# Optimization experiments

Hardware: AMD Instinct MI355X
Metric: run time of the kernel (lower is better)

## Reference

```python
import jax, jax.numpy as jnp
import numpy as np

B, KVH, HPK, D = 4, 8, 4, 128          # batch, n_kv_heads, n_heads_per_kv, head_size
SEQ_KV = 4096                           # cached history length
SEQ = SEQ_KV + 1                        # history + current token
K, LOCAL_K, SINK, RANK = 512, 128, 4, 32


def gather(t, axis, i):
    """Broadcasting take_along_axis, mirroring the torch `gather` helper."""
    axis = axis % t.ndim
    tgt = list(t.shape)
    tgt[axis] = i.shape[axis]
    return jnp.take_along_axis(t, jnp.broadcast_to(i, tgt), axis)


def sparse_q_score(q, key_cpu_t, cur_key_t):
    # q: (B,KVH,HPK,1,D); key_cpu_t: (B,KVH,D,SEQ_KV); cur_key_t: (B,KVH,1,D,1)
    absq = jnp.abs(q).sum(2, keepdims=True)                    # (B,KVH,1,1,D)
    _, idx = jax.lax.top_k(absq, RANK)                         # (B,KVH,1,1,RANK)
    q_proj = gather(q, -1, idx)                                # (B,KVH,HPK,1,RANK)
    idx_t = jnp.swapaxes(idx, -1, -2)                          # (B,KVH,1,RANK,1)
    k_hist = gather(key_cpu_t[:, :, None], -2, idx_t)          # (B,KVH,1,RANK,SEQ_KV)
    k_cur = gather(cur_key_t, -2, idx_t)                       # (B,KVH,1,RANK,1)
    k_proj = jnp.concatenate([k_hist, k_cur], -1)              # (B,KVH,1,RANK,SEQ)
    scale = jnp.sqrt(jnp.abs(q_proj).sum(-1) / jnp.abs(q).sum(-1) * D)[..., None]
    return jnp.matmul(q_proj, k_proj) / scale                  # (B,KVH,HPK,1,SEQ)


def setup_inputs():
    key = jax.random.key(0)
    ks = jax.random.split(key, 6)
    query = jax.random.normal(ks[0], (B, KVH * HPK, 1, D), jnp.float32)
    k = jax.random.normal(ks[1], (B, KVH, 1, D), jnp.float32)
    v = jax.random.normal(ks[2], (B, KVH, 1, D), jnp.float32)
    logmask = jnp.zeros((B, KVH * HPK, 1, SEQ), jnp.float32)
    key_cpu = jax.random.normal(ks[3], (B, KVH, SEQ_KV, D), jnp.float32)
    value_cpu = jax.random.normal(ks[4], (B, KVH, SEQ_KV, D), jnp.float32)
    s_key_cpu = jnp.swapaxes(key_cpu, -1, -2)                  # head-size-contiguous copy
    mean_v = jax.random.normal(ks[5], (B, KVH, 1, 1, D), jnp.float32)
    return {"query": query, "key": k, "value": v, "logmask": logmask,
            "key_cpu": key_cpu, "value_cpu": value_cpu,
            "s_key_cpu": s_key_cpu, "mean_v": mean_v}


def reference(query, key, value, logmask, key_cpu, value_cpu, s_key_cpu, mean_v):
    q = query.reshape(B, KVH, HPK, 1, D)
    k = key.reshape(B, KVH, 1, 1, D)
    v = value.reshape(B, KVH, 1, 1, D)
    lm = logmask.reshape(B, KVH, HPK, 1, SEQ)
    # approximate scores over the full key history + current key
    score = (sparse_q_score(q, s_key_cpu, jnp.swapaxes(k, 3, 4)) + lm).astype(jnp.float32)
    # causal index over history (excluding current token): 0 = most recent unmasked
    neg = jnp.isneginf(lm[..., :-1])
    ci = jnp.where(neg, -1,
                   jnp.cumsum((~neg)[..., ::-1].astype(jnp.int32), -1)[..., ::-1] - 1)
    is_local = (0 <= ci) & (ci < LOCAL_K)
    is_sink = ci >= SEQ - SINK - 1
    fmax = jnp.finfo(jnp.float32).max
    topk_score = jnp.where(is_local | is_sink, fmax, score[..., :-1]).sum(2, keepdims=True)
    kk = min(K + SINK, SEQ)
    _, indices = jax.lax.top_k(topk_score, kk)                 # (B,KVH,1,1,kk)
    # running mean value update
    mean_v_new = (mean_v * (SEQ - 1) + v.astype(jnp.float32)) / SEQ
    # weight reallocation to the mean value
    norm = jax.nn.softmax(score, -1)
    kv_weight = gather(norm, -1, indices).sum(-1) + norm[..., -1]  # (B,KVH,HPK,1)
    # gather selected K/V and append current token
    kv_idx = indices[..., 0, :, None]                          # (B,KVH,1,kk,1)
    key_g = jnp.concatenate([gather(key_cpu[:, :, None], -2, kv_idx), k], -2)   # (B,KVH,1,kk+1,D)
    val_g = jnp.concatenate([gather(value_cpu[:, :, None], -2, kv_idx), v], -2)
    cur_idx = jnp.full(indices.shape[:-1] + (1,), SEQ - 1, indices.dtype)
    lm_g = gather(lm, -1, jnp.concatenate([indices, cur_idx], -1))  # (B,KVH,HPK,1,kk+1)
    # dense attention over the reduced key set
    scores = jnp.matmul(q, jnp.swapaxes(key_g, -1, -2)) * (D ** -0.5) + lm_g
    weights = jax.nn.softmax(scores.astype(jnp.float32), -1) * kv_weight[..., None]
    out = jnp.matmul(weights, val_g) + (1.0 - kv_weight[..., None]) * mean_v_new
    return out.reshape(B, KVH * HPK, 1, D), weights.reshape(B, KVH * HPK, 1, kk + 1)
```

## Files before the change

### kernel.cpp

```cpp
#include <hip/hip_runtime.h>
#include <math.h>

#define NBH 32
#define HPKN 4
#define DN 128
#define SEQKV 4096
#define SEQN 4097
#define SSTR 4100
#define RANKN 32
#define KSEL 516
#define SINKN 4
#define LOCALK 128
#define NMASK 132
#define NTOP 384
#define NCHUNK 16

__global__ __launch_bounds__(256) void k2_scores(
    const float* __restrict__ q, const float* __restrict__ key,
    const float* __restrict__ skey, const float* __restrict__ lm,
    float* __restrict__ scores, float* __restrict__ tk,
    float2* __restrict__ partials) {
  int bh = blockIdx.y;
  int s0 = blockIdx.x << 8;
  int t = threadIdx.x;
  int wave = t >> 6, lane = t & 63;
  __shared__ float qv[4][128];
  __shared__ float absq[128];
  __shared__ int sel[RANKN];
  __shared__ float qp[4][RANKN];
  __shared__ float wred[4][4];

  {
    float v0 = q[(size_t)bh * 512 + t];
    float v1 = q[(size_t)bh * 512 + 256 + t];
    qv[t >> 7][t & 127] = v0;
    qv[2 + (t >> 7)][t & 127] = v1;
  }
  __syncthreads();
  if (t < 128)
    absq[t] = fabsf(qv[0][t]) + fabsf(qv[1][t]) + fabsf(qv[2][t]) + fabsf(qv[3][t]);
  __syncthreads();
  if (t < 128) {
    float a = absq[t];
    int rank = 0;
    for (int e = 0; e < 128; ++e) {
      float ae = absq[e];
      rank += (ae > a) || (ae == a && e < t);
    }
    if (rank < RANKN) sel[rank] = t;
  }
  __syncthreads();
  {
    float fa = fabsf(qv[wave][lane]) + fabsf(qv[wave][lane + 64]);
    for (int off = 32; off > 0; off >>= 1) fa += __shfl_down(fa, off);
    float full = __shfl(fa, 0);
    float qsel = (lane < RANKN) ? qv[wave][sel[lane]] : 0.f;
    float sv = fabsf(qsel);
    for (int off = 32; off > 0; off >>= 1) sv += __shfl_down(sv, off);
    float selsum = __shfl(sv, 0);
    float scale = sqrtf(selsum / full * 128.f);
    if (lane < RANKN) qp[wave][lane] = qsel / scale;
  }
  __syncthreads();

  if (blockIdx.x == 0) {
    float kv = (lane < RANKN) ? key[bh * 128 + sel[lane]] : 0.f;
    float pr = (lane < RANKN) ? qp[wave][lane] * kv : 0.f;
    for (int off = 32; off > 0; off >>= 1) pr += __shfl_down(pr, off);
    if (lane == 0)
      scores[(size_t)(bh * 4 + wave) * SSTR + SEQKV] =
          pr + lm[(size_t)(bh * 4 + wave) * SEQN + SEQKV];
  }

  const float* kb = skey + (size_t)bh * 128 * 4096;
  float a0 = 0, a1 = 0, a2 = 0, a3 = 0;
#pragma unroll 8
  for (int r = 0; r < RANKN; ++r) {
    float k0 = kb[((size_t)sel[r] << 12) + s0 + t];
    a0 += qp[0][r] * k0;
    a1 += qp[1][r] * k0;
    a2 += qp[2][r] * k0;
    a3 += qp[3][r] * k0;
  }
  float sc[4];
  {
    int s = s0 + t;
    sc[0] = a0 + lm[(size_t)(bh * 4 + 0) * SEQN + s];
    sc[1] = a1 + lm[(size_t)(bh * 4 + 1) * SEQN + s];
    sc[2] = a2 + lm[(size_t)(bh * 4 + 2) * SEQN + s];
    sc[3] = a3 + lm[(size_t)(bh * 4 + 3) * SEQN + s];
    float sum = sc[0] + sc[1] + sc[2] + sc[3];
#pragma unroll
    for (int p = 0; p < 4; ++p)
      scores[(size_t)(bh * 4 + p) * SSTR + s] = sc[p];
    tk[(bh << 12) + s] = sum;
  }

#pragma unroll
  for (int p = 0; p < 4; ++p) {
    float mx = sc[p];
    for (int off = 32; off > 0; off >>= 1) mx = fmaxf(mx, __shfl_down(mx, off));
    if (lane == 0) wred[wave][p] = mx;
  }
  __syncthreads();
  float bm[4];
#pragma unroll
  for (int p = 0; p < 4; ++p)
    bm[p] = fmaxf(fmaxf(wred[0][p], wred[1][p]), fmaxf(wred[2][p], wred[3][p]));
  __syncthreads();
#pragma unroll
  for (int p = 0; p < 4; ++p) {
    float e = expf(sc[p] - bm[p]);
    for (int off = 32; off > 0; off >>= 1) e += __shfl_down(e, off);
    if (lane == 0) wred[wave][p] = e;
  }
  __syncthreads();
  if (t < 4) {
    float s = wred[0][t] + wred[1][t] + wred[2][t] + wred[3][t];
    partials[(size_t)(bh * 4 + t) * NCHUNK + blockIdx.x] = make_float2(bm[t], s);
  }
}

__global__ __launch_bounds__(256) void k3_topk(
    const float* __restrict__ tk, int* __restrict__ indices) {
  int bh = blockIdx.x;
  int t = threadIdx.x;
  int lane = t & 63;
  __shared__ unsigned us[4096];
  __shared__ unsigned hist[2048];
  __shared__ unsigned long long binlist[2048];
  __shared__ unsigned long long selk[512];
  __shared__ unsigned chunkSum[32];
  __shared__ int c1, c2, binB_s, nAbove_s, needed_s;

  {
    const float4* tk4 = (const float4*)(tk + (bh << 12));
    for (int i = t; i < 1024; i += 256) {
      float4 v = tk4[i];
      unsigned b0 = __float_as_uint(v.x), b1 = __float_as_uint(v.y);
      unsigned b2 = __float_as_uint(v.z), b3 = __float_as_uint(v.w);
      us[i * 4 + 0] = (b0 & 0x80000000u) ? ~b0 : (b0 | 0x80000000u);
      us[i * 4 + 1] = (b1 & 0x80000000u) ? ~b1 : (b1 | 0x80000000u);
      us[i * 4 + 2] = (b2 & 0x80000000u) ? ~b2 : (b2 | 0x80000000u);
      us[i * 4 + 3] = (b3 & 0x80000000u) ? ~b3 : (b3 | 0x80000000u);
    }
  }
  for (int i = t; i < 2048; i += 256) hist[i] = 0;
  if (t == 0) { c1 = 0; c2 = 0; }
  __syncthreads();

  for (int s = SINKN + t; s < SEQKV - LOCALK; s += 256)
    atomicAdd(&hist[us[s] >> 21], 1u);
  __syncthreads();

  if (t < 32) {
    unsigned sum = 0;
    for (int i = 0; i < 64; ++i) sum += hist[t * 64 + i];
    chunkSum[t] = sum;
  }
  __syncthreads();

  if (t < 64) {
    int l = t;
    unsigned x = (l < 32) ? chunkSum[l] : 0;
    unsigned sfx = x;
    for (int off = 1; off < 64; off <<= 1) {
      unsigned y = __shfl_down(sfx, off);
      if (l + off < 64) sfx += y;
    }
    unsigned above = sfx - x;
    bool hit = (l < 32) && (above < NTOP) && (above + x >= NTOP);
    unsigned long long mask = __ballot(hit);
    int C = __ffsll(mask) - 1;
    unsigned aboveC = __shfl(above, C);
    unsigned h = hist[C * 64 + l];
    unsigned sfx2 = h;
    for (int off = 1; off < 64; off <<= 1) {
      unsigned y = __shfl_down(sfx2, off);
      if (l + off < 64) sfx2 += y;
    }
    unsigned above2 = aboveC + (sfx2 - h);
    bool hit2 = (above2 < NTOP) && (above2 + h >= NTOP);
    unsigned long long mask2 = __ballot(hit2);
    int lB = __ffsll(mask2) - 1;
    if (l == lB) {
      binB_s = C * 64 + l;
      nAbove_s = (int)above2;
      needed_s = NTOP - (int)above2;
    }
  }
  __syncthreads();
  unsigned B = (unsigned)binB_s;
  int nAbove = nAbove_s, needed = needed_s;

  for (int s0 = SINKN; s0 < SEQKV - LOCALK; s0 += 256) {
    int s = s0 + t;
    bool valid = (s < SEQKV - LOCALK);
    unsigned u = valid ? us[s] : 0u;
    unsigned bin = u >> 21;
    bool win = valid && (bin > B);
    bool bnd = valid && (bin == B);
    unsigned long long mw = __ballot(win);
    unsigned long long mb = __ballot(bnd);
    int bw = 0, bb = 0;
    if (lane == 0) {
      if (mw) bw = atomicAdd(&c1, __popcll(mw));
      if (mb) bb = atomicAdd(&c2, __popcll(mb));
    }
    bw = __shfl(bw, 0);
    bb = __shfl(bb, 0);
    unsigned long long lmask = (1ULL << lane) - 1ULL;
    unsigned long long key = ((unsigned long long)u << 32) | (unsigned)(~s);
    if (win) selk[bw + __popcll(mw & lmask)] = key;
    if (bnd) {
      int pos = bb + __popcll(mb & lmask);
      if (pos < 2048) binlist[pos] = key;
    }
  }
  __syncthreads();
  int m2 = c2;
  int p2 = 1;
  while (p2 < m2) p2 <<= 1;
  for (int i = m2 + t; i < p2; i += 256) binlist[i] = 0ULL;
  __syncthreads();
  for (int k = 2; k <= p2; k <<= 1)
    for (int j = k >> 1; j > 0; j >>= 1) {
      for (int i = t; i < p2; i += 256) {
        int ixj = i ^ j;
        if (ixj > i) {
          bool desc = ((i & k) == 0);
          unsigned long long a = binlist[i], bb2 = binlist[ixj];
          if ((a < bb2) == desc) { binlist[i] = bb2; binlist[ixj] = a; }
        }
      }
      __syncthreads();
    }
  for (int i = t; i < needed; i += 256) selk[nAbove + i] = binlist[i];
  for (int i = NTOP + t; i < 512; i += 256) selk[i] = 0ULL;
  __syncthreads();

  unsigned long long e0 = selk[t], e1 = selk[t + 256];
  int i1 = t + 256;
  for (int k = 2; k <= 512; k <<= 1) {
    for (int j = k >> 1; j > 0; j >>= 1) {
      if (j == 256) {
        if (e0 < e1) { unsigned long long tmp = e0; e0 = e1; e1 = tmp; }
      } else if (j >= 64) {
        selk[t] = e0; selk[i1] = e1;
        __syncthreads();
        unsigned long long p0 = selk[t ^ j], p1 = selk[i1 ^ j];
        __syncthreads();
        bool d0 = ((t & k) == 0), l0 = ((t & j) == 0);
        e0 = (d0 == l0) ? (e0 > p0 ? e0 : p0) : (e0 < p0 ? e0 : p0);
        bool d1 = ((i1 & k) == 0), l1 = ((i1 & j) == 0);
        e1 = (d1 == l1) ? (e1 > p1 ? e1 : p1) : (e1 < p1 ? e1 : p1);
      } else {
        unsigned long long p0 = __shfl_xor(e0, j);
        unsigned long long p1 = __shfl_xor(e1, j);
        bool d0 = ((t & k) == 0), l0 = ((t & j) == 0);
        e0 = (d0 == l0) ? (e0 > p0 ? e0 : p0) : (e0 < p0 ? e0 : p0);
        bool d1 = ((i1 & k) == 0);
        e1 = (d1 == l0) ? (e1 > p1 ? e1 : p1) : (e1 < p1 ? e1 : p1);
      }
    }
  }

  if (t < SINKN) indices[bh * KSEL + t] = t;
  for (int i = t; i < LOCALK; i += 256)
    indices[bh * KSEL + SINKN + i] = (SEQKV - LOCALK) + i;
  indices[bh * KSEL + NMASK + t] = (int)(~(unsigned)(e0 & 0xFFFFFFFFu));
  if (t < NTOP - 256)
    indices[bh * KSEL + NMASK + 256 + t] = (int)(~(unsigned)(e1 & 0xFFFFFFFFu));
}

__global__ __launch_bounds__(512) void kC_tail(
    const float* __restrict__ q, const float* __restrict__ key,
    const float* __restrict__ value, const float* __restrict__ lm,
    const float* __restrict__ key_cpu, const float* __restrict__ value_cpu,
    const float* __restrict__ mean_v, const float* __restrict__ scores,
    const float2* __restrict__ partials, const int* __restrict__ indices,
    float* __restrict__ out, float* __restrict__ out_w) {
  const int bh = blockIdx.x;
  const int t = threadIdx.x;
  const int wave = t >> 6, lane = t & 63;
  const int grp = lane >> 4, gl = lane & 15;

  __shared__ int sidxs[520];
  __shared__ float qv[512];
  __shared__ float s2s[4 * 520];
  __shared__ float ws2[4 * 520];
  __shared__ float redA[8], redB[8], redC[8];

  qv[t] = q[((size_t)bh << 9) + t];
  for (int j = t; j < KSEL; j += 512) sidxs[j] = indices[bh * KSEL + j];
  __syncthreads();

  {
    const float rsqd = 0.08838834764831845f;
    const float4* qv4 = (const float4*)qv;
    float4 qA[4], qB[4];
#pragma unroll
    for (int p = 0; p < 4; ++p) {
      qA[p] = qv4[p * 32 + gl * 2];
      qB[p] = qv4[p * 32 + gl * 2 + 1];
    }
    for (int r = 0; r < 17; ++r) {
      int j = (r << 5) + (wave << 2) + grp;
      if (j <= KSEL) {
        int sj = (j < KSEL) ? sidxs[j] : SEQKV;
        const float* krow = (j < KSEL)
            ? key_cpu + ((((size_t)bh << 12) + sj) << 7)
            : key + ((size_t)bh << 7);
        const float4* k4 = (const float4*)krow;
        float4 kA = k4[gl * 2], kB = k4[gl * 2 + 1];
        float d0 = qA[0].x * kA.x + qA[0].y * kA.y + qA[0].z * kA.z + qA[0].w * kA.w +
                   qB[0].x * kB.x + qB[0].y * kB.y + qB[0].z * kB.z + qB[0].w * kB.w;
        float d1 = qA[1].x * kA.x + qA[1].y * kA.y + qA[1].z * kA.z + qA[1].w * kA.w +
                   qB[1].x * kB.x + qB[1].y * kB.y + qB[1].z * kB.z + qB[1].w * kB.w;
        float d2 = qA[2].x * kA.x + qA[2].y * kA.y + qA[2].z * kA.z + qA[2].w * kA.w +
                   qB[2].x * kB.x + qB[2].y * kB.y + qB[2].z * kB.z + qB[2].w * kB.w;
        float d3 = qA[3].x * kA.x + qA[3].y * kA.y + qA[3].z * kA.z + qA[3].w * kA.w +
                   qB[3].x * kB.x + qB[3].y * kB.y + qB[3].z * kB.z + qB[3].w * kB.w;
        for (int off = 8; off > 0; off >>= 1) {
          d0 += __shfl_down(d0, off);
          d1 += __shfl_down(d1, off);
          d2 += __shfl_down(d2, off);
          d3 += __shfl_down(d3, off);
        }
        if (gl == 0) {
          size_t lmb = (size_t)(bh * 4) * SEQN + sj;
          s2s[0 * 520 + j] = d0 * rsqd + lm[lmb + 0 * SEQN];
          s2s[1 * 520 + j] = d1 * rsqd + lm[lmb + 1 * SEQN];
          s2s[2 * 520 + j] = d2 * rsqd + lm[lmb + 2 * SEQN];
          s2s[3 * 520 + j] = d3 * rsqd + lm[lmb + 3 * SEQN];
        }
      }
    }
  }
  __syncthreads();

  const int p = t >> 7, tt = t & 127;
  const int qw = tt >> 6;
  const int bhp = bh * 4 + p;
  float kvw;
  {
    const float* srow = scores + (size_t)bhp * SSTR;
    float cur = srow[SEQKV];

    float m = cur, sumexp;
    {
      float2 pc[NCHUNK];
#pragma unroll
      for (int c = 0; c < NCHUNK; ++c) {
        pc[c] = partials[(size_t)bhp * NCHUNK + c];
        m = fmaxf(m, pc[c].x);
      }
      float s = expf(cur - m);
#pragma unroll
      for (int c = 0; c < NCHUNK; ++c) s += pc[c].y * expf(pc[c].x - m);
      sumexp = s;
    }

    float ss = 0.f;
    for (int j = tt; j < KSEL; j += 128) ss += expf(srow[sidxs[j]] - m);
    for (int off = 32; off > 0; off >>= 1) ss += __shfl_down(ss, off);
    if (lane == 0) redA[p * 2 + qw] = ss;
    __syncthreads();
    float sstot = redA[p * 2] + redA[p * 2 + 1];
    kvw = (sstot + expf(cur - m)) / sumexp;

    float mx = -INFINITY;
    for (int j = tt; j < KSEL + 1; j += 128) mx = fmaxf(mx, s2s[p * 520 + j]);
    for (int off = 32; off > 0; off >>= 1) mx = fmaxf(mx, __shfl_down(mx, off));
    if (lane == 0) redB[p * 2 + qw] = mx;
    __syncthreads();
    float m2 = fmaxf(redB[p * 2], redB[p * 2 + 1]);
    float se = 0.f;
    for (int j = tt; j < KSEL + 1; j += 128) se += expf(s2s[p * 520 + j] - m2);
    for (int off = 32; off > 0; off >>= 1) se += __shfl_down(se, off);
    if (lane == 0) redC[p * 2 + qw] = se;
    __syncthreads();
    float inv = kvw / (redC[p * 2] + redC[p * 2 + 1]);

    for (int j = tt; j < KSEL + 1; j += 128) {
      float w = expf(s2s[p * 520 + j] - m2) * inv;
      ws2[p * 520 + j] = w;
      out_w[(size_t)bhp * (KSEL + 1) + j] = w;
    }
  }
  __syncthreads();

  {
    const int d = tt;
    float vcur = value[((size_t)bh << 7) + d];
    float mvn = (mean_v[((size_t)bh << 7) + d] * 4096.f + vcur) / 4097.f;
    float a0 = (1.f - kvw) * mvn, a1 = 0.f, a2 = 0.f, a3 = 0.f;
    const float* vbase = value_cpu + ((size_t)bh << 19);
    for (int j = 0; j < KSEL; j += 4) {
      int s0 = sidxs[j], s1 = sidxs[j + 1], s2i = sidxs[j + 2], s3 = sidxs[j + 3];
      a0 += ws2[p * 520 + j] * vbase[((size_t)s0 << 7) + d];
      a1 += ws2[p * 520 + j + 1] * vbase[((size_t)s1 << 7) + d];
      a2 += ws2[p * 520 + j + 2] * vbase[((size_t)s2i << 7) + d];
      a3 += ws2[p * 520 + j + 3] * vbase[((size_t)s3 << 7) + d];
    }
    a0 += ws2[p * 520 + KSEL] * vcur;
    out[((size_t)bhp << 7) + d] = (a0 + a1) + (a2 + a3);
  }
}

extern "C" void kernel_launch(void* const* d_in, const int* in_sizes, int n_in,
                              void* d_out, int out_size, void* d_ws, size_t ws_size,
                              hipStream_t stream) {
  const float* query     = (const float*)d_in[0];
  const float* key       = (const float*)d_in[1];
  const float* value     = (const float*)d_in[2];
  const float* logmask   = (const float*)d_in[3];
  const float* key_cpu   = (const float*)d_in[4];
  const float* value_cpu = (const float*)d_in[5];
  const float* s_key_cpu = (const float*)d_in[6];
  const float* mean_v    = (const float*)d_in[7];

  float* out   = (float*)d_out;
  float* out_w = out + 16384;

  char* ws = (char*)d_ws;
  int*    indices  = (int*)(ws + 20480);
  float*  scores   = (float*)(ws + 86528);
  float*  tk       = (float*)(ws + 2185728);
  float2* partials = (float2*)(ws + 3242496);

  hipLaunchKernelGGL(k2_scores, dim3(NCHUNK, NBH), dim3(256), 0, stream,
                     query, key, s_key_cpu, logmask, scores, tk, partials);
  hipLaunchKernelGGL(k3_topk, dim3(NBH), dim3(256), 0, stream,
                     tk, indices);
  hipLaunchKernelGGL(kC_tail, dim3(NBH), dim3(512), 0, stream,
                     query, key, value, logmask, key_cpu, value_cpu,
                     mean_v, scores, partials, indices, out, out_w);
}
```

Measured before the change: 258.1 us.

## Split tail attention across key chunks with last-block combine via atomic counter

The tail kernel previously ran one 512-thread block per (batch, kv-head), serially gathering 516 selected keys and values. It now splits the selected keys into 8 chunks per head. Each chunk computes local scores, a local softmax max/sum and a partial PV product into workspace, and the last block to finish, detected with an atomic counter reset in the first kernel, merges the partials and writes the outputs. This raises parallelism from 32 blocks to 256 to hide gather latency, at the cost of extra workspace traffic, atomics and a serialized final combine step.

New measurement: 254.2 us. About the same (-1.5%).

```diff
diff --git a/kernel.cpp b/kernel.cpp
--- a/kernel.cpp
+++ b/kernel.cpp
@@ -14,12 +14,14 @@
 #define NMASK 132
 #define NTOP 384
 #define NCHUNK 16
+#define NCH2 8
+#define NJC 65
 
 __global__ __launch_bounds__(256) void k2_scores(
     const float* __restrict__ q, const float* __restrict__ key,
     const float* __restrict__ skey, const float* __restrict__ lm,
     float* __restrict__ scores, float* __restrict__ tk,
-    float2* __restrict__ partials) {
+    float2* __restrict__ partials, int* __restrict__ ctrB) {
   int bh = blockIdx.y;
   int s0 = blockIdx.x << 8;
   int t = threadIdx.x;
@@ -29,6 +31,8 @@
   __shared__ int sel[RANKN];
   __shared__ float qp[4][RANKN];
   __shared__ float wred[4][4];
+
+  if (blockIdx.x == 0 && t == 0) ctrB[bh] = 0;
 
   {
     float v0 = q[(size_t)bh * 512 + t];
@@ -273,30 +277,44 @@
     indices[bh * KSEL + NMASK + 256 + t] = (int)(~(unsigned)(e1 & 0xFFFFFFFFu));
 }
 
-__global__ __launch_bounds__(512) void kC_tail(
+__global__ __launch_bounds__(256) void kB_tail(
     const float* __restrict__ q, const float* __restrict__ key,
     const float* __restrict__ value, const float* __restrict__ lm,
     const float* __restrict__ key_cpu, const float* __restrict__ value_cpu,
     const float* __restrict__ mean_v, const float* __restrict__ scores,
     const float2* __restrict__ partials, const int* __restrict__ indices,
+    float* __restrict__ pv, float2* __restrict__ pms,
+    float* __restrict__ s2_g, int* __restrict__ ctrB,
     float* __restrict__ out, float* __restrict__ out_w) {
-  const int bh = blockIdx.x;
+  const int bh = blockIdx.y;
+  const int c = blockIdx.x;
   const int t = threadIdx.x;
   const int wave = t >> 6, lane = t & 63;
-  const int grp = lane >> 4, gl = lane & 15;
-
-  __shared__ int sidxs[520];
+
   __shared__ float qv[512];
-  __shared__ float s2s[4 * 520];
-  __shared__ float ws2[4 * 520];
-  __shared__ float redA[8], redB[8], redC[8];
+  __shared__ int sidx[NJC];
+  __shared__ float s2[4][NJC];
+  __shared__ float we[4][NJC];
+  __shared__ float mred[4], sred[4];
+  __shared__ int sidxAll[KSEL];
+  __shared__ float ef[NCH2 * 4];
+  __shared__ float mm[4], sg[4], kvws[4];
+  __shared__ int lastFlag;
+
+  const int j0 = c * NJC;
+  const int nj = min(NJC, KSEL + 1 - j0);
 
   qv[t] = q[((size_t)bh << 9) + t];
-  for (int j = t; j < KSEL; j += 512) sidxs[j] = indices[bh * KSEL + j];
+  qv[t + 256] = q[((size_t)bh << 9) + t + 256];
+  if (t < nj) {
+    int j = j0 + t;
+    sidx[t] = (j < KSEL) ? indices[bh * KSEL + j] : -1;
+  }
   __syncthreads();
 
   {
     const float rsqd = 0.08838834764831845f;
+    const int grp = t >> 4, gl = t & 15;
     const float4* qv4 = (const float4*)qv;
     float4 qA[4], qB[4];
 #pragma unroll
@@ -304,23 +322,24 @@
       qA[p] = qv4[p * 32 + gl * 2];
       qB[p] = qv4[p * 32 + gl * 2 + 1];
     }
-    for (int r = 0; r < 17; ++r) {
-      int j = (r << 5) + (wave << 2) + grp;
-      if (j <= KSEL) {
-        int sj = (j < KSEL) ? sidxs[j] : SEQKV;
-        const float* krow = (j < KSEL)
+#pragma unroll
+    for (int r = 0; r < 5; ++r) {
+      int jl = grp + (r << 4);
+      if (jl < nj) {
+        int sj = sidx[jl];
+        const float* krow = (sj >= 0)
             ? key_cpu + ((((size_t)bh << 12) + sj) << 7)
             : key + ((size_t)bh << 7);
         const float4* k4 = (const float4*)krow;
-        float4 kA = k4[gl * 2], kB = k4[gl * 2 + 1];
+        float4 kA = k4[gl * 2], kB4 = k4[gl * 2 + 1];
         float d0 = qA[0].x * kA.x + qA[0].y * kA.y + qA[0].z * kA.z + qA[0].w * kA.w +
-                   qB[0].x * kB.x + qB[0].y * kB.y + qB[0].z * kB.z + qB[0].w * kB.w;
+                   qB[0].x * kB4.x + qB[0].y * kB4.y + qB[0].z * kB4.z + qB[0].w * kB4.w;
         float d1 = qA[1].x * kA.x + qA[1].y * kA.y + qA[1].z * kA.z + qA[1].w * kA.w +
-                   qB[1].x * kB.x + qB[1].y * kB.y + qB[1].z * kB.z + qB[1].w * kB.w;
+                   qB[1].x * kB4.x + qB[1].y * kB4.y + qB[1].z * kB4.z + qB[1].w * kB4.w;
         float d2 = qA[2].x * kA.x + qA[2].y * kA.y + qA[2].z * kA.z + qA[2].w * kA.w +
-                   qB[2].x * kB.x + qB[2].y * kB.y + qB[2].z * kB.z + qB[2].w * kB.w;
+                   qB[2].x * kB4.x + qB[2].y * kB4.y + qB[2].z * kB4.z + qB[2].w * kB4.w;
         float d3 = qA[3].x * kA.x + qA[3].y * kA.y + qA[3].z * kA.z + qA[3].w * kA.w +
-                   qB[3].x * kB.x + qB[3].y * kB.y + qB[3].z * kB.z + qB[3].w * kB.w;
+                   qB[3].x * kB4.x + qB[3].y * kB4.y + qB[3].z * kB4.z + qB[3].w * kB4.w;
         for (int off = 8; off > 0; off >>= 1) {
           d0 += __shfl_down(d0, off);
           d1 += __shfl_down(d1, off);
@@ -328,83 +347,122 @@
           d3 += __shfl_down(d3, off);
         }
         if (gl == 0) {
-          size_t lmb = (size_t)(bh * 4) * SEQN + sj;
-          s2s[0 * 520 + j] = d0 * rsqd + lm[lmb + 0 * SEQN];
-          s2s[1 * 520 + j] = d1 * rsqd + lm[lmb + 1 * SEQN];
-          s2s[2 * 520 + j] = d2 * rsqd + lm[lmb + 2 * SEQN];
-          s2s[3 * 520 + j] = d3 * rsqd + lm[lmb + 3 * SEQN];
+          int s = (sj >= 0) ? sj : SEQKV;
+          size_t lmb = (size_t)(bh * 4) * SEQN + s;
+          s2[0][jl] = d0 * rsqd + lm[lmb + 0 * SEQN];
+          s2[1][jl] = d1 * rsqd + lm[lmb + 1 * SEQN];
+          s2[2][jl] = d2 * rsqd + lm[lmb + 2 * SEQN];
+          s2[3][jl] = d3 * rsqd + lm[lmb + 3 * SEQN];
         }
       }
     }
   }
   __syncthreads();
 
-  const int p = t >> 7, tt = t & 127;
-  const int qw = tt >> 6;
-  const int bhp = bh * 4 + p;
-  float kvw;
-  {
+  {
+    const int p = wave;
+    float va = (lane < nj) ? s2[p][lane] : -INFINITY;
+    float vb = (lane + 64 < nj) ? s2[p][lane + 64] : -INFINITY;
+    float mx = fmaxf(va, vb);
+    for (int off = 32; off > 0; off >>= 1) mx = fmaxf(mx, __shfl_down(mx, off));
+    mx = __shfl(mx, 0);
+    float ea = (lane < nj) ? expf(va - mx) : 0.f;
+    float eb = (lane + 64 < nj) ? expf(vb - mx) : 0.f;
+    if (lane < nj) we[p][lane] = ea;
+    if (lane + 64 < nj) we[p][lane + 64] = eb;
+    float su = ea + eb;
+    for (int off = 32; off > 0; off >>= 1) su += __shfl_down(su, off);
+    if (lane == 0) { mred[p] = mx; sred[p] = su; }
+  }
+  __syncthreads();
+
+  {
+    const int d = t & 127, pp = t >> 7;
+    float a0 = 0.f, a1 = 0.f;
+    for (int jl = 0; jl < nj; ++jl) {
+      int sj = sidx[jl];
+      const float* vrow = (sj >= 0)
+          ? value_cpu + ((((size_t)bh << 12) + sj) << 7)
+          : value + ((size_t)bh << 7);
+      float v = vrow[d];
+      a0 += we[pp][jl] * v;
+      a1 += we[pp + 2][jl] * v;
+    }
+    int base = (bh * NCH2 + c) * 4;
+    pv[(size_t)(base + pp) * 128 + d] = a0;
+    pv[(size_t)(base + pp + 2) * 128 + d] = a1;
+    if (t < 4) pms[base + t] = make_float2(mred[t], sred[t]);
+  }
+  if (t < nj) {
+#pragma unroll
+    for (int p = 0; p < 4; ++p)
+      s2_g[(size_t)(bh * 4 + p) * 520 + j0 + t] = s2[p][t];
+  }
+
+  __threadfence();
+  __syncthreads();
+  if (t == 0) lastFlag = (atomicAdd(&ctrB[bh], 1) == NCH2 - 1);
+  __syncthreads();
+  if (!lastFlag) return;
+  __threadfence();
+
+  for (int jj = t; jj < KSEL; jj += 256) sidxAll[jj] = indices[bh * KSEL + jj];
+  __syncthreads();
+
+  {
+    const int p = wave;
+    const int bhp = bh * 4 + p;
+    float2 mp = (lane < NCH2) ? pms[(bh * NCH2 + lane) * 4 + p]
+                              : make_float2(-INFINITY, 0.f);
+    float m2 = mp.x;
+    for (int off = 32; off > 0; off >>= 1) m2 = fmaxf(m2, __shfl_down(m2, off));
+    m2 = __shfl(m2, 0);
+    float sig = (lane < NCH2) ? mp.y * expf(mp.x - m2) : 0.f;
+    for (int off = 32; off > 0; off >>= 1) sig += __shfl_down(sig, off);
+    sig = __shfl(sig, 0);
+    if (lane < NCH2) ef[lane * 4 + p] = expf(mp.x - m2);
+
     const float* srow = scores + (size_t)bhp * SSTR;
     float cur = srow[SEQKV];
-
-    float m = cur, sumexp;
-    {
-      float2 pc[NCHUNK];
-#pragma unroll
-      for (int c = 0; c < NCHUNK; ++c) {
-        pc[c] = partials[(size_t)bhp * NCHUNK + c];
-        m = fmaxf(m, pc[c].x);
-      }
-      float s = expf(cur - m);
-#pragma unroll
-      for (int c = 0; c < NCHUNK; ++c) s += pc[c].y * expf(pc[c].x - m);
-      sumexp = s;
-    }
-
-    float ss = 0.f;
-    for (int j = tt; j < KSEL; j += 128) ss += expf(srow[sidxs[j]] - m);
-    for (int off = 32; off > 0; off >>= 1) ss += __shfl_down(ss, off);
-    if (lane == 0) redA[p * 2 + qw] = ss;
-    __syncthreads();
-    float sstot = redA[p * 2] + redA[p * 2 + 1];
-    kvw = (sstot + expf(cur - m)) / sumexp;
-
-    float mx = -INFINITY;
-    for (int j = tt; j < KSEL + 1; j += 128) mx = fmaxf(mx, s2s[p * 520 + j]);
-    for (int off = 32; off > 0; off >>= 1) mx = fmaxf(mx, __shfl_down(mx, off));
-    if (lane == 0) redB[p * 2 + qw] = mx;
-    __syncthreads();
-    float m2 = fmaxf(redB[p * 2], redB[p * 2 + 1]);
-    float se = 0.f;
-    for (int j = tt; j < KSEL + 1; j += 128) se += expf(s2s[p * 520 + j] - m2);
-    for (int off = 32; off > 0; off >>= 1) se += __shfl_down(se, off);
-    if (lane == 0) redC[p * 2 + qw] = se;
-    __syncthreads();
-    float inv = kvw / (redC[p * 2] + redC[p * 2 + 1]);
-
-    for (int j = tt; j < KSEL + 1; j += 128) {
-      float w = expf(s2s[p * 520 + j] - m2) * inv;
-      ws2[p * 520 + j] = w;
-      out_w[(size_t)bhp * (KSEL + 1) + j] = w;
-    }
-  }
-  __syncthreads();
-
-  {
-    const int d = tt;
+    float2 pc = (lane < NCHUNK) ? partials[(size_t)bhp * NCHUNK + lane]
+                                : make_float2(-INFINITY, 0.f);
+    float mA = fmaxf(pc.x, cur);
+    for (int off = 32; off > 0; off >>= 1) mA = fmaxf(mA, __shfl_down(mA, off));
+    mA = __shfl(mA, 0);
+    float sA = (lane < NCHUNK) ? pc.y * expf(pc.x - mA) : 0.f;
+    for (int off = 32; off > 0; off >>= 1) sA += __shfl_down(sA, off);
+    sA = __shfl(sA, 0) + expf(cur - mA);
+    float selm = 0.f;
+    for (int jj = lane; jj < KSEL; jj += 64) selm += expf(srow[sidxAll[jj]] - mA);
+    for (int off = 32; off > 0; off >>= 1) selm += __shfl_down(selm, off);
+    selm = __shfl(selm, 0);
+    float kvw = (selm + expf(cur - mA)) / sA;
+    if (lane == 0) { mm[p] = m2; sg[p] = sig; kvws[p] = kvw; }
+  }
+  __syncthreads();
+
+#pragma unroll
+  for (int p = 0; p < 4; ++p) {
+    float scl = kvws[p] / sg[p], mmp = mm[p];
+    const float* s2r = s2_g + (size_t)(bh * 4 + p) * 520;
+    for (int jj = t; jj < KSEL + 1; jj += 256)
+      out_w[(size_t)(bh * 4 + p) * (KSEL + 1) + jj] = expf(s2r[jj] - mmp) * scl;
+  }
+
+  {
+    const int d = t & 127, pp = t >> 7;
     float vcur = value[((size_t)bh << 7) + d];
     float mvn = (mean_v[((size_t)bh << 7) + d] * 4096.f + vcur) / 4097.f;
-    float a0 = (1.f - kvw) * mvn, a1 = 0.f, a2 = 0.f, a3 = 0.f;
-    const float* vbase = value_cpu + ((size_t)bh << 19);
-    for (int j = 0; j < KSEL; j += 4) {
-      int s0 = sidxs[j], s1 = sidxs[j + 1], s2i = sidxs[j + 2], s3 = sidxs[j + 3];
-      a0 += ws2[p * 520 + j] * vbase[((size_t)s0 << 7) + d];
-      a1 += ws2[p * 520 + j + 1] * vbase[((size_t)s1 << 7) + d];
-      a2 += ws2[p * 520 + j + 2] * vbase[((size_t)s2i << 7) + d];
-      a3 += ws2[p * 520 + j + 3] * vbase[((size_t)s3 << 7) + d];
-    }
-    a0 += ws2[p * 520 + KSEL] * vcur;
-    out[((size_t)bhp << 7) + d] = (a0 + a1) + (a2 + a3);
+#pragma unroll
+    for (int pi = 0; pi < 2; ++pi) {
+      int p = pp + pi * 2;
+      float acc = 0.f;
+#pragma unroll
+      for (int c2 = 0; c2 < NCH2; ++c2)
+        acc += pv[(size_t)((bh * NCH2 + c2) * 4 + p) * 128 + d] * ef[c2 * 4 + p];
+      out[(size_t)(bh * 4 + p) * 128 + d] =
+          acc * kvws[p] / sg[p] + (1.f - kvws[p]) * mvn;
+    }
   }
 }
 
@@ -424,16 +482,21 @@
   float* out_w = out + 16384;
 
   char* ws = (char*)d_ws;
+  int*    ctrB     = (int*)(ws + 0);
+  float2* pms      = (float2*)(ws + 128);
   int*    indices  = (int*)(ws + 20480);
   float*  scores   = (float*)(ws + 86528);
   float*  tk       = (float*)(ws + 2185728);
+  float*  pv       = (float*)(ws + 2185728);
+  float*  s2_g     = (float*)(ws + 2710016);
   float2* partials = (float2*)(ws + 3242496);
 
   hipLaunchKernelGGL(k2_scores, dim3(NCHUNK, NBH), dim3(256), 0, stream,
-                     query, key, s_key_cpu, logmask, scores, tk, partials);
+                     query, key, s_key_cpu, logmask, scores, tk, partials, ctrB);
   hipLaunchKernelGGL(k3_topk, dim3(NBH), dim3(256), 0, stream,
                      tk, indices);
-  hipLaunchKernelGGL(kC_tail, dim3(NBH), dim3(512), 0, stream,
+  hipLaunchKernelGGL(kB_tail, dim3(NCH2, NBH), dim3(256), 0, stream,
                      query, key, value, logmask, key_cpu, value_cpu,
-                     mean_v, scores, partials, indices, out, out_w);
+                     mean_v, scores, partials, indices,
+                     pv, pms, s2_g, ctrB, out, out_w);
 }
```
